# Kernel optimization log

Hardware: AMD Instinct MI355X
Metric: run time of the kernel (lower is better)

Reference implementation:

```python
import jax, jax.numpy as jnp
import numpy as np

SCORE_THRESH = 0.05
IOU_THRESH = 0.5
TOP_K = 1000      # candidates fed to NMS
MAX_DET = 100     # padded output detections


def _build_anchors(H, W):
    """Standard RetinaNet anchors: levels P3..P7, 3 ratios x 3 scales."""
    ratios = np.array([0.5, 1.0, 2.0])
    scales = np.array([2 ** 0, 2 ** (1.0 / 3.0), 2 ** (2.0 / 3.0)])
    all_anchors = []
    for lvl in [3, 4, 5, 6, 7]:
        stride = 2 ** lvl
        base_size = 2 ** (lvl + 2)
        # 9 base anchors centered at origin (ratio-major, scale-minor ordering)
        s = base_size * np.tile(scales, len(ratios))          # [9]
        r = np.repeat(ratios, len(scales))                    # [9]
        areas = s * s
        w = np.sqrt(areas / r)
        h = w * r
        base = np.stack([-w / 2, -h / 2, w / 2, h / 2], axis=1)  # [9,4]
        fh = (H + stride - 1) // stride
        fw = (W + stride - 1) // stride
        sx = (np.arange(fw) + 0.5) * stride
        sy = (np.arange(fh) + 0.5) * stride
        gx, gy = np.meshgrid(sx, sy)
        shifts = np.stack([gx.ravel(), gy.ravel(), gx.ravel(), gy.ravel()], axis=1)  # [fh*fw,4]
        all_anchors.append((shifts[:, None, :] + base[None, :, :]).reshape(-1, 4))
    return np.concatenate(all_anchors, axis=0).astype(np.float32)  # [A,4]


def setup_inputs() -> dict:
    key = jax.random.key(0)
    k1, k2 = jax.random.split(key)
    H = W = 1024
    C = 80
    anchors = jnp.asarray(_build_anchors(H, W))[None]            # [1,A,4]
    A = anchors.shape[1]
    classifications = jax.random.uniform(k1, (1, A, C), dtype=jnp.float32)
    regressions = jax.random.normal(k2, (1, A, 4), dtype=jnp.float32)
    return {"classifications": classifications, "regressions": regressions,
            "anchors": anchors, "img_h": H, "img_w": W}


def _decode_clip(anchors, regressions, img_h, img_w):
    # BBoxTransform with mean 0, std [0.1,0.1,0.2,0.2]
    aw = anchors[..., 2] - anchors[..., 0]
    ah = anchors[..., 3] - anchors[..., 1]
    acx = anchors[..., 0] + 0.5 * aw
    acy = anchors[..., 1] + 0.5 * ah
    dx = regressions[..., 0] * 0.1
    dy = regressions[..., 1] * 0.1
    dw = regressions[..., 2] * 0.2
    dh = regressions[..., 3] * 0.2
    pcx = acx + dx * aw
    pcy = acy + dy * ah
    pw = jnp.exp(dw) * aw
    ph = jnp.exp(dh) * ah
    boxes = jnp.stack([pcx - 0.5 * pw, pcy - 0.5 * ph,
                       pcx + 0.5 * pw, pcy + 0.5 * ph], axis=-1)
    # ClipBoxes
    lo = jnp.zeros(4, boxes.dtype)
    hi = jnp.array([img_w, img_h, img_w, img_h], boxes.dtype)
    return jnp.clip(boxes, lo, hi)  # [1,A,4]


def _nms_keep(boxes, valid):
    """Sequential greedy NMS over score-sorted boxes [K,4]; returns keep mask [K]."""
    K = boxes.shape[0]
    areas = jnp.maximum(boxes[:, 2] - boxes[:, 0], 0) * jnp.maximum(boxes[:, 3] - boxes[:, 1], 0)
    idx = jnp.arange(K)

    def body(i, keep):
        b = boxes[i]
        xx1 = jnp.maximum(b[0], boxes[:, 0])
        yy1 = jnp.maximum(b[1], boxes[:, 1])
        xx2 = jnp.minimum(b[2], boxes[:, 2])
        yy2 = jnp.minimum(b[3], boxes[:, 3])
        inter = jnp.maximum(xx2 - xx1, 0) * jnp.maximum(yy2 - yy1, 0)
        iou = inter / (areas[i] + areas - inter + 1e-8)
        suppress = (iou > IOU_THRESH) & (idx > i)
        return jnp.where(keep[i], keep & ~suppress, keep)

    return jax.lax.fori_loop(0, K, body, valid)


def reference(classifications, regressions, anchors, img_h, img_w):
    boxes = _decode_clip(anchors, regressions, img_h, img_w)       # [1,A,4]
    scores = jnp.max(classifications, axis=2)                      # [1,A]
    # Score threshold: mask out low scores, keep fixed shape (padded NMS)
    s0 = jnp.where(scores[0] > SCORE_THRESH, scores[0], -1.0)      # [A]
    top_scores, top_idx = jax.lax.top_k(s0, TOP_K)                 # sorted desc
    cand_boxes = boxes[0, top_idx]                                 # [K,4]
    keep = _nms_keep(cand_boxes, top_scores > SCORE_THRESH)        # [K]
    final = jnp.where(keep, top_scores, -1.0)
    det_scores, sel = jax.lax.top_k(final, MAX_DET)                # [100]
    det_idx = top_idx[sel]                                         # indices into A
    det_valid = det_scores > SCORE_THRESH
    cls = classifications[0, det_idx]                              # [100,C]
    nms_scores = jnp.where(det_valid, jnp.max(cls, axis=1), 0.0)
    nms_class = jnp.where(det_valid, jnp.argmax(cls, axis=1), -1)
    det_boxes = jnp.where(det_valid[:, None], boxes[0, det_idx], 0.0)
    return (nms_scores, nms_class, det_boxes)
```

## Files before the change

### kernel.cpp

```cpp
#include <hip/hip_runtime.h>
#include <stdint.h>

#define SCORE_THRESH 0.05f
#define IOU_THRESH 0.5f
#define TOP_K 1000
#define MAX_DET 100

#define D0_BITS 13
#define D0_BINS 8192
#define NREP 4
#define CAND_CAP 2048

typedef unsigned int u32;
typedef unsigned long long u64;

#define OFF_HIST0    0
#define OFF_HIST1    131072
#define OFF_STATE    393216
#define OFF_BAR      394240
#define MEMSET_LEN   427008
#define OFF_CAND     427008
#define OFF_RFLAG    435200
#define OFF_SIDX     439200
#define OFF_SSCORE   443200
#define OFF_CBOX     447200
#define OFF_M        463200
#define OFF_SCORES   591200

#define BAR_STRIDE_U32 1024

__device__ __forceinline__ u32 order_f32(float f) {
    u32 b = __float_as_uint(f);
    return (b & 0x80000000u) ? ~b : (b | 0x80000000u);
}

__device__ __forceinline__ void st_sc(u32* p, u32 v)   { __hip_atomic_store(p, v, __ATOMIC_RELAXED, __HIP_MEMORY_SCOPE_AGENT); }
__device__ __forceinline__ void st_sc(float* p, float v){ __hip_atomic_store(p, v, __ATOMIC_RELAXED, __HIP_MEMORY_SCOPE_AGENT); }
__device__ __forceinline__ void st_sc(u64* p, u64 v)   { __hip_atomic_store(p, v, __ATOMIC_RELAXED, __HIP_MEMORY_SCOPE_AGENT); }
__device__ __forceinline__ u32  ld_sc(u32* p)          { return __hip_atomic_load(p, __ATOMIC_RELAXED, __HIP_MEMORY_SCOPE_AGENT); }

__device__ __forceinline__ void gbar(u32* barr, int k, int b, u32 G, bool dowait) {
    __syncthreads();
    if (threadIdx.x == 0) {
        asm volatile("s_waitcnt vmcnt(0)" ::: "memory");
        u32* base = barr + (size_t)k * BAR_STRIDE_U32;
        int g = b & 7;
        u32 gsz = G >> 3;
        if (__hip_atomic_fetch_add(base + g * 32, 1u, __ATOMIC_RELAXED,
                                   __HIP_MEMORY_SCOPE_AGENT) == gsz - 1u) {
            if (__hip_atomic_fetch_add(base + 8 * 32, 1u, __ATOMIC_RELAXED,
                                       __HIP_MEMORY_SCOPE_AGENT) == 7u) {
                #pragma unroll
                for (int g2 = 0; g2 < 8; g2++)
                    st_sc(base + (16 + g2) * 32, 1u);
            }
        }
        if (dowait) {
            while (ld_sc(base + (16 + g) * 32) == 0u)
                __builtin_amdgcn_s_sleep(32);
        }
        asm volatile("" ::: "memory");
    }
    __syncthreads();
}

union ShMem {
    u32 hl[D0_BINS / 2];
    u32 wtot[4];
    struct { u32 wcnt[4]; u32 wbase[4]; u32 bbase; } cmp;
    struct { u64 ckeys[8]; u32 wpart[4][8]; } rank;
    struct {
        u64 Ml[256 * 16];
        u64 keepS[16];
        u32 nib[256];
        int act[TOP_K];
        u32 wsum[4];
        int nactS;
        int det[MAX_DET];
    } nms;
};

__global__ void __launch_bounds__(256, 2)
mega(const float* __restrict__ cls, const float* __restrict__ regs,
     const float* __restrict__ anchors, const int* __restrict__ pH,
     const int* __restrict__ pW, int A, int C,
     char* __restrict__ ws, float* __restrict__ out)
{
    __shared__ ShMem sh;
    u32*   hist0  = (u32*)(ws + OFF_HIST0);
    u32*   hist1  = (u32*)(ws + OFF_HIST1);
    u32*   state  = (u32*)(ws + OFF_STATE);
    u32*   barr   = (u32*)(ws + OFF_BAR);
    u32*   cand   = (u32*)(ws + OFF_CAND);
    u32*   rflag  = (u32*)(ws + OFF_RFLAG);
    u32*   sidx   = (u32*)(ws + OFF_SIDX);
    float* sscore = (float*)(ws + OFF_SSCORE);
    float* cbox   = (float*)(ws + OFF_CBOX);
    u64*   M      = (u64*)(ws + OFF_M);
    float* scores = (float*)(ws + OFF_SCORES);

    const int t = threadIdx.x;
    const int b = blockIdx.x;
    const int G = gridDim.x;
    const int gid = b * 256 + t;
    const int gstride = G * 256;
    const int lane = t & 63, wv = t >> 6;

    if (C == 80) {
        for (int i = t; i < D0_BINS / 2; i += 256) sh.hl[i] = 0;
        __syncthreads();
        int sub = t & 3;
        int la  = t >> 2;
        int nstrips = (A + 63) >> 6;
        int per = (nstrips + G - 1) / G;
        for (int s = 0; s < per; s++) {
            int a = (b * per + s) * 64 + la;
            float m = -1e30f;
            if (a < A) {
                const float* p = cls + (size_t)a * 80 + sub * 4;
                #pragma unroll
                for (int k2 = 0; k2 < 5; k2++) {
                    float4 v = *(const float4*)(p + k2 * 16);
                    m = fmaxf(m, fmaxf(fmaxf(v.x, v.y), fmaxf(v.z, v.w)));
                }
            }
            m = fmaxf(m, __shfl_xor(m, 1, 64));
            m = fmaxf(m, __shfl_xor(m, 2, 64));
            if (sub == 0 && a < A) {
                float s0 = (m > SCORE_THRESH) ? m : -1.0f;
                st_sc(&scores[a], s0);
                u32 d = order_f32(s0) >> (32 - D0_BITS);
                atomicAdd(&sh.hl[d >> 1], (d & 1) ? 0x10000u : 1u);
            }
        }
        __syncthreads();
        u32* rep = hist0 + (size_t)(b & (NREP - 1)) * D0_BINS;
        for (int i = t; i < D0_BINS / 2; i += 256) {
            u32 v = sh.hl[i];
            if (v & 0xFFFFu) atomicAdd(&rep[2 * i],     v & 0xFFFFu);
            if (v >> 16)     atomicAdd(&rep[2 * i + 1], v >> 16);
        }
    } else {
        u32* rep = hist0 + (size_t)(b & (NREP - 1)) * D0_BINS;
        for (int a = gid; a < A; a += gstride) {
            const float* p = cls + (size_t)a * C;
            float m = -1e30f;
            for (int c = 0; c < C; c++) m = fmaxf(m, p[c]);
            float s0 = (m > SCORE_THRESH) ? m : -1.0f;
            st_sc(&scores[a], s0);
            atomicAdd(&rep[order_f32(s0) >> (32 - D0_BITS)], 1u);
        }
    }
    gbar(barr, 0, b, (u32)G, b == 0);

    if (b == 0) {
        u32 cnt[32];
        #pragma unroll
        for (int i = 0; i < 32; i++) cnt[i] = 0;
        const uint4* hp = (const uint4*)hist0;
        #pragma unroll
        for (int r = 0; r < NREP; r++) {
            #pragma unroll
            for (int i = 0; i < 8; i++) {
                uint4 v = hp[r * (D0_BINS / 4) + t * 8 + i];
                cnt[4*i]   += v.x; cnt[4*i+1] += v.y;
                cnt[4*i+2] += v.z; cnt[4*i+3] += v.w;
            }
        }
        u32 s = 0;
        #pragma unroll
        for (int i = 0; i < 32; i++) s += cnt[i];
        u32 x = s;
        for (int off = 1; off < 64; off <<= 1) {
            u32 v = (u32)__shfl_down((int)x, off, 64);
            if (lane + off < 64) x += v;
        }
        if (lane == 0) sh.wtot[wv] = x;
        __syncthreads();
        u32 above = x - s;
        for (int w = wv + 1; w < 4; w++) above += sh.wtot[w];
        if (above < TOP_K && above + s >= TOP_K) {
            u32 cum = above;
            for (int i = 31; i >= 0; i--) {
                cum += cnt[i];
                if (cum >= TOP_K) {
                    st_sc(&state[1 * 32], (u32)(t * 32 + i));
                    st_sc(&state[0 * 32], TOP_K - (cum - cnt[i]));
                    break;
                }
            }
        }
    }
    gbar(barr, 1, b, (u32)G, true);

    {
        u32 d0cut = state[1 * 32];
        for (int a = gid; a < A; a += gstride) {
            u32 key = order_f32(scores[a]);
            if ((key >> (32 - D0_BITS)) == d0cut)
                atomicAdd(&hist1[(key >> 3) & 0xFFFFu], 1u);
        }
    }
    gbar(barr, 2, b, (u32)G, b == 0);

    if (b == 0) {
        u32 k = state[0 * 32];
        const uint4* hp = (const uint4*)hist1;
        u32 chk[8]; u32 s = 0;
        #pragma unroll
        for (int c = 0; c < 8; c++) {
            u32 cs = 0;
            #pragma unroll
            for (int i = 0; i < 8; i++) {
                uint4 v = hp[t * 64 + c * 8 + i];
                cs += v.x + v.y + v.z + v.w;
            }
            chk[c] = cs; s += cs;
        }
        u32 x = s;
        for (int off = 1; off < 64; off <<= 1) {
            u32 v = (u32)__shfl_down((int)x, off, 64);
            if (lane + off < 64) x += v;
        }
        if (lane == 0) sh.wtot[wv] = x;
        __syncthreads();
        u32 above = x - s;
        for (int w = wv + 1; w < 4; w++) above += sh.wtot[w];
        if (above < k && above + s >= k) {
            u32 cum = above;
            bool done = false;
            for (int c = 7; c >= 0 && !done; c--) {
                if (cum + chk[c] >= k) {
                    for (int i = 7; i >= 0 && !done; i--) {
                        uint4 v = hp[t * 64 + c * 8 + i];
                        u32 vv[4] = {v.x, v.y, v.z, v.w};
                        for (int q = 3; q >= 0 && !done; q--) {
                            cum += vv[q];
                            if (cum >= k) {
                                st_sc(&state[2 * 32], (u32)(t * 256 + c * 32 + i * 4 + q));
                                done = true;
                            }
                        }
                    }
                } else cum += chk[c];
            }
        }
    }
    gbar(barr, 3, b, (u32)G, true);

    {
        u32 cut = (state[1 * 32] << 16) | state[2 * 32];
        int nr = (A + gstride - 1) / gstride;
        for (int r = 0; r < nr; r++) {
            int a = gid + r * gstride;
            bool pass = (a < A) && ((order_f32(scores[a]) >> 3) >= cut);
            u64 mask = __ballot(pass ? 1 : 0);
            if (lane == 0) sh.cmp.wcnt[wv] = (u32)__popcll(mask);
            __syncthreads();
            if (t == 0) {
                u32 s = 0;
                #pragma unroll
                for (int w = 0; w < 4; w++) { sh.cmp.wbase[w] = s; s += sh.cmp.wcnt[w]; }
                sh.cmp.bbase = s ? atomicAdd(&state[5 * 32], s) : 0u;
            }
            __syncthreads();
            if (pass) {
                u32 pos = sh.cmp.bbase + sh.cmp.wbase[wv]
                        + (u32)__popcll(mask & ((1ull << lane) - 1ull));
                if (pos < CAND_CAP) st_sc(&cand[pos], (u32)a);
            }
            __syncthreads();
        }
    }
    gbar(barr, 4, b, (u32)G, b < CAND_CAP / 8);

    {
        int n = (int)state[5 * 32]; if (n > CAND_CAP) n = CAND_CAP;
        for (int bb = b; bb < CAND_CAP / 8; bb += G) {
            u64 kj[8];
            #pragma unroll
            for (int q = 0; q < 8; q++) {
                int j = t * 8 + q;
                u64 kk = 0ull;
                if (j < n) {
                    u32 a = cand[j];
                    kk = ((u64)order_f32(scores[a]) << 32) | (u64)(0xFFFFFFFFu - a);
                }
                kj[q] = kk;
            }
            if (t < 8) {
                int c = bb * 8 + t;
                u64 ck = 0ull;
                if (c < n) {
                    u32 a = cand[c];
                    ck = ((u64)order_f32(scores[a]) << 32) | (u64)(0xFFFFFFFFu - a);
                }
                sh.rank.ckeys[t] = ck;
            }
            __syncthreads();
            u64 ck[8];
            #pragma unroll
            for (int q = 0; q < 8; q++) ck[q] = sh.rank.ckeys[q];
            u32 cnt8[8] = {0,0,0,0,0,0,0,0};
            #pragma unroll
            for (int q = 0; q < 8; q++) {
                u64 kq = kj[q];
                #pragma unroll
                for (int q2 = 0; q2 < 8; q2++) cnt8[q2] += (kq > ck[q2]) ? 1u : 0u;
            }
            #pragma unroll
            for (int q2 = 0; q2 < 8; q2++) {
                u32 x = cnt8[q2];
                x += (u32)__shfl_xor((int)x, 1, 64);
                x += (u32)__shfl_xor((int)x, 2, 64);
                x += (u32)__shfl_xor((int)x, 4, 64);
                x += (u32)__shfl_xor((int)x, 8, 64);
                x += (u32)__shfl_xor((int)x, 16, 64);
                x += (u32)__shfl_xor((int)x, 32, 64);
                if (lane == 0) sh.rank.wpart[wv][q2] = x;
            }
            __syncthreads();
            if (t < 8) {
                int c = bb * 8 + t;
                if (c < n) {
                    u32 rank = sh.rank.wpart[0][t] + sh.rank.wpart[1][t]
                             + sh.rank.wpart[2][t] + sh.rank.wpart[3][t];
                    if (rank < TOP_K) {
                        u32 a = cand[c];
                        st_sc(&sidx[rank], a);
                        st_sc(&sscore[rank], scores[a]);
                        float4 an = *(const float4*)(anchors + (size_t)a * 4);
                        float4 rg = *(const float4*)(regs + (size_t)a * 4);
                        float aw = an.z - an.x, ah = an.w - an.y;
                        float acx = an.x + 0.5f * aw, acy = an.y + 0.5f * ah;
                        float pcx = acx + (rg.x * 0.1f) * aw;
                        float pcy = acy + (rg.y * 0.1f) * ah;
                        float pw = expf(rg.z * 0.2f) * aw;
                        float ph = expf(rg.w * 0.2f) * ah;
                        float W = (float)(*pW), H = (float)(*pH);
                        st_sc(&cbox[rank * 4 + 0], fminf(fmaxf(pcx - 0.5f * pw, 0.0f), W));
                        st_sc(&cbox[rank * 4 + 1], fminf(fmaxf(pcy - 0.5f * ph, 0.0f), H));
                        st_sc(&cbox[rank * 4 + 2], fminf(fmaxf(pcx + 0.5f * pw, 0.0f), W));
                        st_sc(&cbox[rank * 4 + 3], fminf(fmaxf(pcy + 0.5f * ph, 0.0f), H));
                    }
                }
            }
            __syncthreads();
        }
    }
    gbar(barr, 5, b, (u32)G, b * 4 < TOP_K);

    {
        const float4* B4 = (const float4*)cbox;
        for (int i = b * 4 + wv; i < TOP_K; i += G * 4) {
            float4 bi = B4[i];
            float ai = fmaxf(bi.z - bi.x, 0.0f) * fmaxf(bi.w - bi.y, 0.0f);
            u64 any = 0ull;
            for (int w = 0; w < 16; w++) {
                int j = w * 64 + lane;
                bool sup = false;
                if (j < TOP_K && j > i) {
                    float4 bj = B4[j];
                    float aj = fmaxf(bj.z - bj.x, 0.0f) * fmaxf(bj.w - bj.y, 0.0f);
                    float xx1 = fmaxf(bi.x, bj.x), yy1 = fmaxf(bi.y, bj.y);
                    float xx2 = fminf(bi.z, bj.z), yy2 = fminf(bi.w, bj.w);
                    float inter = fmaxf(xx2 - xx1, 0.0f) * fmaxf(yy2 - yy1, 0.0f);
                    float iou = inter / (ai + aj - inter + 1e-8f);
                    sup = iou > IOU_THRESH;
                }
                u64 mask = __ballot(sup ? 1 : 0);
                if (lane == 0) { st_sc(&M[(size_t)i * 16 + w], mask); any |= mask; }
            }
            if (lane == 0) st_sc(&rflag[i], (any != 0ull) ? 1u : 0u);
        }
    }
    gbar(barr, 6, b, (u32)G, b == 0);

    if (b == 0) {
        {
            u32 nb = 0;
            int j0 = 4 * t;
            #pragma unroll
            for (int q = 0; q < 4; q++) {
                int j = j0 + q;
                if (j < TOP_K && sscore[j] > SCORE_THRESH) nb |= (1u << q);
            }
            sh.nms.nib[t] = nb;
        }
        u32 flags = 0; int cnt = 0;
        {
            int r0 = 4 * t;
            #pragma unroll
            for (int q = 0; q < 4; q++) {
                int r = r0 + q;
                if (r < TOP_K && rflag[r]) { flags |= (1u << q); cnt++; }
            }
        }
        int x = cnt;
        for (int off = 1; off < 64; off <<= 1) {
            int v = __shfl_up(x, off, 64);
            if (lane >= off) x += v;
        }
        if (lane == 63) sh.nms.wsum[wv] = (u32)x;
        __syncthreads();
        if (t < 16) {
            u64 w = 0;
            for (int m2 = 0; m2 < 16; m2++)
                w |= ((u64)sh.nms.nib[t * 16 + m2]) << (4 * m2);
            sh.nms.keepS[t] = w;
        }
        int base = 0;
        for (int w = 0; w < wv; w++) base += (int)sh.nms.wsum[w];
        int pos = base + x - cnt;
        {
            int r0 = 4 * t;
            #pragma unroll
            for (int q = 0; q < 4; q++)
                if (flags & (1u << q)) sh.nms.act[pos++] = r0 + q;
        }
        if (t == 0) {
            int na = 0;
            for (int w = 0; w < 4; w++) na += (int)sh.nms.wsum[w];
            sh.nms.nactS = na;
        }
        __syncthreads();
        int nact = sh.nms.nactS;

        for (int c0 = 0; c0 < nact; c0 += 256) {
            int cn = (nact - c0 < 256) ? (nact - c0) : 256;
            for (int i = t; i < cn * 16; i += 256) {
                int row = sh.nms.act[c0 + (i >> 4)];
                sh.nms.Ml[i] = M[(size_t)row * 16 + (i & 15)];
            }
            __syncthreads();
            if (wv == 0) {
                u64 kp = (lane < 16) ? sh.nms.keepS[lane] : 0ull;
                for (int k = 0; k < cn; k++) {
                    int i = sh.nms.act[c0 + k];
                    u64 kw = __shfl(kp, i >> 6, 64);
                    if ((kw >> (i & 63)) & 1ull) {
                        u64 m2 = (lane < 16) ? sh.nms.Ml[k * 16 + lane] : 0ull;
                        kp &= ~m2;
                    }
                }
                if (lane < 16) sh.nms.keepS[lane] = kp;
            }
            __syncthreads();
        }

        if (t == 0) {
            int cnt2 = 0;
            for (int w = 0; w < 16 && cnt2 < MAX_DET; w++) {
                u64 kw = sh.nms.keepS[w];
                while (kw && cnt2 < MAX_DET) {
                    int bbit = __ffsll((unsigned long long)kw) - 1;
                    sh.nms.det[cnt2++] = w * 64 + bbit;
                    kw &= kw - 1;
                }
            }
            for (; cnt2 < MAX_DET; cnt2++) sh.nms.det[cnt2] = -1;
        }
        __syncthreads();
        if (t < MAX_DET) {
            int i = sh.nms.det[t];
            if (i >= 0) {
                u32 a = sidx[i];
                const float* p = cls + (size_t)a * C;
                float best = -1e30f; int bc = 0;
                if (C == 80) {
                    #pragma unroll
                    for (int c4 = 0; c4 < 20; c4++) {
                        float4 v = *(const float4*)(p + c4 * 4);
                        if (v.x > best) { best = v.x; bc = c4 * 4; }
                        if (v.y > best) { best = v.y; bc = c4 * 4 + 1; }
                        if (v.z > best) { best = v.z; bc = c4 * 4 + 2; }
                        if (v.w > best) { best = v.w; bc = c4 * 4 + 3; }
                    }
                } else {
                    best = p[0]; bc = 0;
                    for (int c = 1; c < C; c++) {
                        float v = p[c];
                        if (v > best) { best = v; bc = c; }
                    }
                }
                out[t] = best;
                out[MAX_DET + t] = (float)bc;
                out[2 * MAX_DET + t * 4 + 0] = cbox[i * 4 + 0];
                out[2 * MAX_DET + t * 4 + 1] = cbox[i * 4 + 1];
                out[2 * MAX_DET + t * 4 + 2] = cbox[i * 4 + 2];
                out[2 * MAX_DET + t * 4 + 3] = cbox[i * 4 + 3];
            } else {
                out[t] = 0.0f;
                out[MAX_DET + t] = -1.0f;
                out[2 * MAX_DET + t * 4 + 0] = 0.0f;
                out[2 * MAX_DET + t * 4 + 1] = 0.0f;
                out[2 * MAX_DET + t * 4 + 2] = 0.0f;
                out[2 * MAX_DET + t * 4 + 3] = 0.0f;
            }
        }
    }
}

extern "C" void kernel_launch(void* const* d_in, const int* in_sizes, int n_in,
                              void* d_out, int out_size, void* d_ws, size_t ws_size,
                              hipStream_t stream) {
    (void)n_in; (void)out_size; (void)ws_size;
    const float* cls     = (const float*)d_in[0];
    const float* regs    = (const float*)d_in[1];
    const float* anchors = (const float*)d_in[2];
    const int*   pH      = (const int*)d_in[3];
    const int*   pW      = (const int*)d_in[4];
    int A = in_sizes[1] / 4;
    int C = in_sizes[0] / A;

    static int nCU = 0;
    if (nCU <= 0) {
        int dev = 0;
        hipGetDevice(&dev);
        hipDeviceGetAttribute(&nCU, hipDeviceAttributeMultiprocessorCount, dev);
        if (nCU <= 0) nCU = 256;
    }
    int G = (2 * nCU) & ~7;
    if (G < 8) G = 8;

    char* ws = (char*)d_ws;
    hipMemsetAsync(ws, 0, MEMSET_LEN, stream);
    mega<<<dim3(G), dim3(256), 0, stream>>>(cls, regs, anchors, pH, pW, A, C,
                                            ws, (float*)d_out);
}
```

Before: 181.5 us.

## Retire most blocks after the first phase and run later phases on 64 survivor blocks

After the score/histogram phase, only the first 64 blocks keep going. All later grid barriers count only these survivors and their grid-stride loops use the smaller stride. This cuts the cost of barriers across hundreds of blocks, and the barrier spin sleep is also shortened. Survivors also pre-touch the scores array during the radix-select step, and the candidate key load is hoisted out of the per-rank loop. In exchange, the later scans over the full anchor array run with much less parallelism.

Result: slower. 212.3 us (+17.0%).

```diff
diff --git a/kernel.cpp b/kernel.cpp
--- a/kernel.cpp
+++ b/kernel.cpp
@@ -10,6 +10,7 @@
 #define D0_BINS 8192
 #define NREP 4
 #define CAND_CAP 2048
+#define NSURV 64
 
 typedef unsigned int u32;
 typedef unsigned long long u64;
@@ -39,13 +40,12 @@
 __device__ __forceinline__ void st_sc(u64* p, u64 v)   { __hip_atomic_store(p, v, __ATOMIC_RELAXED, __HIP_MEMORY_SCOPE_AGENT); }
 __device__ __forceinline__ u32  ld_sc(u32* p)          { return __hip_atomic_load(p, __ATOMIC_RELAXED, __HIP_MEMORY_SCOPE_AGENT); }
 
-__device__ __forceinline__ void gbar(u32* barr, int k, int b, u32 G, bool dowait) {
+__device__ __forceinline__ void gbar(u32* barr, int k, int b, u32 gsz, bool dowait) {
     __syncthreads();
     if (threadIdx.x == 0) {
         asm volatile("s_waitcnt vmcnt(0)" ::: "memory");
         u32* base = barr + (size_t)k * BAR_STRIDE_U32;
         int g = b & 7;
-        u32 gsz = G >> 3;
         if (__hip_atomic_fetch_add(base + g * 32, 1u, __ATOMIC_RELAXED,
                                    __HIP_MEMORY_SCOPE_AGENT) == gsz - 1u) {
             if (__hip_atomic_fetch_add(base + 8 * 32, 1u, __ATOMIC_RELAXED,
@@ -57,7 +57,7 @@
         }
         if (dowait) {
             while (ld_sc(base + (16 + g) * 32) == 0u)
-                __builtin_amdgcn_s_sleep(32);
+                __builtin_amdgcn_s_sleep(8);
         }
         asm volatile("" ::: "memory");
     }
@@ -146,12 +146,18 @@
             const float* p = cls + (size_t)a * C;
             float m = -1e30f;
             for (int c = 0; c < C; c++) m = fmaxf(m, p[c]);
-            float s0 = (m > SCORE_THRESH) ? m : -1.0f;
-            st_sc(&scores[a], s0);
-            atomicAdd(&rep[order_f32(s0) >> (32 - D0_BITS)], 1u);
-        }
-    }
-    gbar(barr, 0, b, (u32)G, b == 0);
+            st_sc(&scores[a], (m > SCORE_THRESH) ? m : -1.0f);
+            atomicAdd(&rep[order_f32((m > SCORE_THRESH) ? m : -1.0f) >> (32 - D0_BITS)], 1u);
+        }
+    }
+    {
+        bool surv = (b < NSURV);
+        gbar(barr, 0, b, (u32)(G / 8), surv);
+        if (!surv) return;
+    }
+
+    const int gid2 = b * 256 + t;
+    const int gstride2 = NSURV * 256;
 
     if (b == 0) {
         u32 cnt[32];
@@ -191,17 +197,22 @@
             }
         }
     }
-    gbar(barr, 1, b, (u32)G, true);
+    {
+        float acc = 0.0f;
+        for (int a = gid2; a < A; a += gstride2) acc += scores[a];
+        asm volatile("" :: "v"(acc));
+    }
+    gbar(barr, 1, b, NSURV / 8, true);
 
     {
         u32 d0cut = state[1 * 32];
-        for (int a = gid; a < A; a += gstride) {
+        for (int a = gid2; a < A; a += gstride2) {
             u32 key = order_f32(scores[a]);
             if ((key >> (32 - D0_BITS)) == d0cut)
                 atomicAdd(&hist1[(key >> 3) & 0xFFFFu], 1u);
         }
     }
-    gbar(barr, 2, b, (u32)G, b == 0);
+    gbar(barr, 2, b, NSURV / 8, b == 0);
 
     if (b == 0) {
         u32 k = state[0 * 32];
@@ -246,13 +257,13 @@
             }
         }
     }
-    gbar(barr, 3, b, (u32)G, true);
+    gbar(barr, 3, b, NSURV / 8, true);
 
     {
         u32 cut = (state[1 * 32] << 16) | state[2 * 32];
-        int nr = (A + gstride - 1) / gstride;
+        int nr = (A + gstride2 - 1) / gstride2;
         for (int r = 0; r < nr; r++) {
-            int a = gid + r * gstride;
+            int a = gid2 + r * gstride2;
             bool pass = (a < A) && ((order_f32(scores[a]) >> 3) >= cut);
             u64 mask = __ballot(pass ? 1 : 0);
             if (lane == 0) sh.cmp.wcnt[wv] = (u32)__popcll(mask);
@@ -272,22 +283,22 @@
             __syncthreads();
         }
     }
-    gbar(barr, 4, b, (u32)G, b < CAND_CAP / 8);
+    gbar(barr, 4, b, NSURV / 8, true);
 
     {
         int n = (int)state[5 * 32]; if (n > CAND_CAP) n = CAND_CAP;
-        for (int bb = b; bb < CAND_CAP / 8; bb += G) {
-            u64 kj[8];
-            #pragma unroll
-            for (int q = 0; q < 8; q++) {
-                int j = t * 8 + q;
-                u64 kk = 0ull;
-                if (j < n) {
-                    u32 a = cand[j];
-                    kk = ((u64)order_f32(scores[a]) << 32) | (u64)(0xFFFFFFFFu - a);
-                }
-                kj[q] = kk;
-            }
+        u64 kj[8];
+        #pragma unroll
+        for (int q = 0; q < 8; q++) {
+            int j = t * 8 + q;
+            u64 kk = 0ull;
+            if (j < n) {
+                u32 a = cand[j];
+                kk = ((u64)order_f32(scores[a]) << 32) | (u64)(0xFFFFFFFFu - a);
+            }
+            kj[q] = kk;
+        }
+        for (int bb = b; bb < CAND_CAP / 8; bb += NSURV) {
             if (t < 8) {
                 int c = bb * 8 + t;
                 u64 ck = 0ull;
@@ -348,11 +359,11 @@
             __syncthreads();
         }
     }
-    gbar(barr, 5, b, (u32)G, b * 4 < TOP_K);
+    gbar(barr, 5, b, NSURV / 8, true);
 
     {
         const float4* B4 = (const float4*)cbox;
-        for (int i = b * 4 + wv; i < TOP_K; i += G * 4) {
+        for (int i = b * 4 + wv; i < TOP_K; i += NSURV * 4) {
             float4 bi = B4[i];
             float ai = fmaxf(bi.z - bi.x, 0.0f) * fmaxf(bi.w - bi.y, 0.0f);
             u64 any = 0ull;
@@ -374,7 +385,7 @@
             if (lane == 0) st_sc(&rflag[i], (any != 0ull) ? 1u : 0u);
         }
     }
-    gbar(barr, 6, b, (u32)G, b == 0);
+    gbar(barr, 6, b, NSURV / 8, b == 0);
 
     if (b == 0) {
         {
@@ -521,7 +532,7 @@
         if (nCU <= 0) nCU = 256;
     }
     int G = (2 * nCU) & ~7;
-    if (G < 8) G = 8;
+    if (G < NSURV) G = NSURV;
 
     char* ws = (char*)d_ws;
     hipMemsetAsync(ws, 0, MEMSET_LEN, stream);
```

## Double-buffer NMS mask chunks and hoist per-iteration syncs out of compaction loop

Applied to the files above, without the earlier changes.

The serial NMS sweep in block 0 now uses double-buffered 128-row mask chunks, with waves 1-3 prefetching the next chunk while wave 0 runs the suppression scan, and the keep bits stay in registers across chunks. Stream compaction first counts passing elements per thread and reserves one global offset per block, which removes the three block-wide syncs per loop iteration. Other changes: all blocks now wait at barrier 0 and prewarm the score array in cache, the candidate keys are loaded once outside the rank loop, and the barrier spin sleep is shortened. The trade-offs are more global polling traffic and an extra pass over scores.

Result: no change. 180.9 us (-0.4%).

```diff
diff --git a/kernel.cpp b/kernel.cpp
--- a/kernel.cpp
+++ b/kernel.cpp
@@ -10,6 +10,7 @@
 #define D0_BINS 8192
 #define NREP 4
 #define CAND_CAP 2048
+#define NMS_CHUNK 128
 
 typedef unsigned int u32;
 typedef unsigned long long u64;
@@ -39,13 +40,12 @@
 __device__ __forceinline__ void st_sc(u64* p, u64 v)   { __hip_atomic_store(p, v, __ATOMIC_RELAXED, __HIP_MEMORY_SCOPE_AGENT); }
 __device__ __forceinline__ u32  ld_sc(u32* p)          { return __hip_atomic_load(p, __ATOMIC_RELAXED, __HIP_MEMORY_SCOPE_AGENT); }
 
-__device__ __forceinline__ void gbar(u32* barr, int k, int b, u32 G, bool dowait) {
+__device__ __forceinline__ void gbar(u32* barr, int k, int b, u32 gsz, bool dowait) {
     __syncthreads();
     if (threadIdx.x == 0) {
         asm volatile("s_waitcnt vmcnt(0)" ::: "memory");
         u32* base = barr + (size_t)k * BAR_STRIDE_U32;
         int g = b & 7;
-        u32 gsz = G >> 3;
         if (__hip_atomic_fetch_add(base + g * 32, 1u, __ATOMIC_RELAXED,
                                    __HIP_MEMORY_SCOPE_AGENT) == gsz - 1u) {
             if (__hip_atomic_fetch_add(base + 8 * 32, 1u, __ATOMIC_RELAXED,
@@ -57,7 +57,7 @@
         }
         if (dowait) {
             while (ld_sc(base + (16 + g) * 32) == 0u)
-                __builtin_amdgcn_s_sleep(32);
+                __builtin_amdgcn_s_sleep(8);
         }
         asm volatile("" ::: "memory");
     }
@@ -70,7 +70,7 @@
     struct { u32 wcnt[4]; u32 wbase[4]; u32 bbase; } cmp;
     struct { u64 ckeys[8]; u32 wpart[4][8]; } rank;
     struct {
-        u64 Ml[256 * 16];
+        u64 Ml[2 * NMS_CHUNK * 16];
         u64 keepS[16];
         u32 nib[256];
         int act[TOP_K];
@@ -105,6 +105,7 @@
     const int gid = b * 256 + t;
     const int gstride = G * 256;
     const int lane = t & 63, wv = t >> 6;
+    const u32 gsz = (u32)(G >> 3);
 
     if (C == 80) {
         for (int i = t; i < D0_BINS / 2; i += 256) sh.hl[i] = 0;
@@ -151,7 +152,7 @@
             atomicAdd(&rep[order_f32(s0) >> (32 - D0_BITS)], 1u);
         }
     }
-    gbar(barr, 0, b, (u32)G, b == 0);
+    gbar(barr, 0, b, gsz, true);
 
     if (b == 0) {
         u32 cnt[32];
@@ -190,8 +191,12 @@
                 }
             }
         }
-    }
-    gbar(barr, 1, b, (u32)G, true);
+    } else {
+        float acc = 0.0f;
+        for (int a = gid; a < A; a += gstride) acc += scores[a];
+        asm volatile("" :: "v"(acc));
+    }
+    gbar(barr, 1, b, gsz, true);
 
     {
         u32 d0cut = state[1 * 32];
@@ -201,7 +206,7 @@
                 atomicAdd(&hist1[(key >> 3) & 0xFFFFu], 1u);
         }
     }
-    gbar(barr, 2, b, (u32)G, b == 0);
+    gbar(barr, 2, b, gsz, b == 0);
 
     if (b == 0) {
         u32 k = state[0 * 32];
@@ -246,48 +251,60 @@
             }
         }
     }
-    gbar(barr, 3, b, (u32)G, true);
+    gbar(barr, 3, b, gsz, true);
 
     {
         u32 cut = (state[1 * 32] << 16) | state[2 * 32];
         int nr = (A + gstride - 1) / gstride;
+        u32 mycnt = 0;
+        for (int r = 0; r < nr; r++) {
+            int a = gid + r * gstride;
+            mycnt += ((a < A) && ((order_f32(scores[a]) >> 3) >= cut)) ? 1u : 0u;
+        }
+        u32 wc = mycnt;
+        wc += (u32)__shfl_xor((int)wc, 1, 64);
+        wc += (u32)__shfl_xor((int)wc, 2, 64);
+        wc += (u32)__shfl_xor((int)wc, 4, 64);
+        wc += (u32)__shfl_xor((int)wc, 8, 64);
+        wc += (u32)__shfl_xor((int)wc, 16, 64);
+        wc += (u32)__shfl_xor((int)wc, 32, 64);
+        if (lane == 0) sh.cmp.wcnt[wv] = wc;
+        __syncthreads();
+        if (t == 0) {
+            u32 s = 0;
+            #pragma unroll
+            for (int w = 0; w < 4; w++) { sh.cmp.wbase[w] = s; s += sh.cmp.wcnt[w]; }
+            sh.cmp.bbase = s ? atomicAdd(&state[5 * 32], s) : 0u;
+        }
+        __syncthreads();
+        u32 off = sh.cmp.bbase + sh.cmp.wbase[wv];
         for (int r = 0; r < nr; r++) {
             int a = gid + r * gstride;
             bool pass = (a < A) && ((order_f32(scores[a]) >> 3) >= cut);
             u64 mask = __ballot(pass ? 1 : 0);
-            if (lane == 0) sh.cmp.wcnt[wv] = (u32)__popcll(mask);
-            __syncthreads();
-            if (t == 0) {
-                u32 s = 0;
-                #pragma unroll
-                for (int w = 0; w < 4; w++) { sh.cmp.wbase[w] = s; s += sh.cmp.wcnt[w]; }
-                sh.cmp.bbase = s ? atomicAdd(&state[5 * 32], s) : 0u;
-            }
-            __syncthreads();
             if (pass) {
-                u32 pos = sh.cmp.bbase + sh.cmp.wbase[wv]
-                        + (u32)__popcll(mask & ((1ull << lane) - 1ull));
+                u32 pos = off + (u32)__popcll(mask & ((1ull << lane) - 1ull));
                 if (pos < CAND_CAP) st_sc(&cand[pos], (u32)a);
             }
-            __syncthreads();
-        }
-    }
-    gbar(barr, 4, b, (u32)G, b < CAND_CAP / 8);
-
-    {
+            off += (u32)__popcll(mask);
+        }
+    }
+    gbar(barr, 4, b, gsz, b < CAND_CAP / 8);
+
+    if (b < CAND_CAP / 8) {
         int n = (int)state[5 * 32]; if (n > CAND_CAP) n = CAND_CAP;
+        u64 kj[8];
+        #pragma unroll
+        for (int q = 0; q < 8; q++) {
+            int j = t * 8 + q;
+            u64 kk = 0ull;
+            if (j < n) {
+                u32 a = cand[j];
+                kk = ((u64)order_f32(scores[a]) << 32) | (u64)(0xFFFFFFFFu - a);
+            }
+            kj[q] = kk;
+        }
         for (int bb = b; bb < CAND_CAP / 8; bb += G) {
-            u64 kj[8];
-            #pragma unroll
-            for (int q = 0; q < 8; q++) {
-                int j = t * 8 + q;
-                u64 kk = 0ull;
-                if (j < n) {
-                    u32 a = cand[j];
-                    kk = ((u64)order_f32(scores[a]) << 32) | (u64)(0xFFFFFFFFu - a);
-                }
-                kj[q] = kk;
-            }
             if (t < 8) {
                 int c = bb * 8 + t;
                 u64 ck = 0ull;
@@ -348,7 +365,7 @@
             __syncthreads();
         }
     }
-    gbar(barr, 5, b, (u32)G, b * 4 < TOP_K);
+    gbar(barr, 5, b, gsz, b * 4 < TOP_K);
 
     {
         const float4* B4 = (const float4*)cbox;
@@ -374,7 +391,7 @@
             if (lane == 0) st_sc(&rflag[i], (any != 0ull) ? 1u : 0u);
         }
     }
-    gbar(barr, 6, b, (u32)G, b == 0);
+    gbar(barr, 6, b, gsz, b == 0);
 
     if (b == 0) {
         {
@@ -425,28 +442,44 @@
         }
         __syncthreads();
         int nact = sh.nms.nactS;
-
-        for (int c0 = 0; c0 < nact; c0 += 256) {
-            int cn = (nact - c0 < 256) ? (nact - c0) : 256;
-            for (int i = t; i < cn * 16; i += 256) {
-                int row = sh.nms.act[c0 + (i >> 4)];
+        int nchunks = (nact + NMS_CHUNK - 1) / NMS_CHUNK;
+
+        if (nchunks > 0) {
+            int cn0 = (nact < NMS_CHUNK) ? nact : NMS_CHUNK;
+            for (int i = t; i < cn0 * 16; i += 256) {
+                int row = sh.nms.act[i >> 4];
                 sh.nms.Ml[i] = M[(size_t)row * 16 + (i & 15)];
             }
-            __syncthreads();
+        }
+        __syncthreads();
+        u64 kp = (wv == 0 && lane < 16) ? sh.nms.keepS[lane] : 0ull;
+        for (int ci = 0; ci < nchunks; ci++) {
+            int c0 = ci * NMS_CHUNK;
+            int cn = (nact - c0 < NMS_CHUNK) ? (nact - c0) : NMS_CHUNK;
+            int cur = (ci & 1) * (NMS_CHUNK * 16);
+            if (ci + 1 < nchunks && t >= 64) {
+                int c0n = c0 + NMS_CHUNK;
+                int cnn = (nact - c0n < NMS_CHUNK) ? (nact - c0n) : NMS_CHUNK;
+                int nxt = ((ci + 1) & 1) * (NMS_CHUNK * 16);
+                for (int i = t - 64; i < cnn * 16; i += 192) {
+                    int row = sh.nms.act[c0n + (i >> 4)];
+                    sh.nms.Ml[nxt + i] = M[(size_t)row * 16 + (i & 15)];
+                }
+            }
             if (wv == 0) {
-                u64 kp = (lane < 16) ? sh.nms.keepS[lane] : 0ull;
                 for (int k = 0; k < cn; k++) {
                     int i = sh.nms.act[c0 + k];
                     u64 kw = __shfl(kp, i >> 6, 64);
                     if ((kw >> (i & 63)) & 1ull) {
-                        u64 m2 = (lane < 16) ? sh.nms.Ml[k * 16 + lane] : 0ull;
+                        u64 m2 = (lane < 16) ? sh.nms.Ml[cur + k * 16 + lane] : 0ull;
                         kp &= ~m2;
                     }
                 }
-                if (lane < 16) sh.nms.keepS[lane] = kp;
             }
             __syncthreads();
         }
+        if (wv == 0 && lane < 16) sh.nms.keepS[lane] = kp;
+        __syncthreads();
 
         if (t == 0) {
             int cnt2 = 0;
```
